# Kernel tuning notes

Measured on AMD Instinct MI355X. Metric: run time of the kernel, lower is better.

The kernel has to match this reference:

```python
import jax, jax.numpy as jnp
import numpy as np

N_SRC = 100000
N_DST = 100000
N_EDGES = 640000
D = 128
D_OUT = 128


def setup_inputs() -> dict:
    key = jax.random.key(0)
    k1, k2, k3, k4, k5, k6 = jax.random.split(key, 6)
    h_src = jax.random.normal(k1, (N_SRC, D), dtype=jnp.float32)
    h_dst = jax.random.normal(k2, (N_DST, D), dtype=jnp.float32)
    src_idx = jax.random.randint(k3, (N_EDGES,), 0, N_SRC, dtype=jnp.int32)
    dst_idx = jax.random.randint(k4, (N_EDGES,), 0, N_DST, dtype=jnp.int32)
    W = jax.random.normal(k5, (2 * D, D_OUT), dtype=jnp.float32) * 0.05
    b = jax.random.normal(k6, (D_OUT,), dtype=jnp.float32) * 0.05
    return {"h_src": h_src, "h_dst": h_dst, "src_idx": src_idx,
            "dst_idx": dst_idx, "W": W, "b": b}


def reference(h_src, h_dst, src_idx, dst_idx, W, b):
    # copy_u: gather source features along edges -> [E, D]
    msgs = h_src[src_idx]
    # mean aggregation per destination node (segment mean)
    summed = jax.ops.segment_sum(msgs, dst_idx, num_segments=N_DST)  # [N_dst, D]
    deg = jax.ops.segment_sum(jnp.ones((N_EDGES,), dtype=h_src.dtype),
                              dst_idx, num_segments=N_DST)  # [N_dst]
    h_N = summed / jnp.maximum(deg, 1.0)[:, None]
    # concat self + neighbor mean, then linear projection
    h_total = jnp.concatenate([h_dst, h_N], axis=1)  # [N_dst, 2D]
    return h_total @ W + b
```

## Files before the change

kernel.cpp:

```cpp
#include <hip/hip_runtime.h>

#define D 128
#define N_SRC 100000
#define N_DST 100000
#define N_EDGES 640000

#define SCAN_BLK 1024
#define N_SCAN_BLOCKS ((N_DST + SCAN_BLK - 1) / SCAN_BLK)

typedef __attribute__((ext_vector_type(8))) short s8v;
typedef __attribute__((ext_vector_type(4))) float f32x4;

__device__ __forceinline__ unsigned short f2bf(float f) {
    unsigned int u = __float_as_uint(f);
    u += 0x7fffu + ((u >> 16) & 1u);
    return (unsigned short)(u >> 16);
}


__global__ __launch_bounds__(256) void hist_kernel(
    const int* __restrict__ dst_idx, int* __restrict__ counts)
{
    int e = blockIdx.x * 256 + threadIdx.x;
    if (e < N_EDGES) atomicAdd(&counts[dst_idx[e]], 1);
}

__global__ __launch_bounds__(256) void scan_blocks(
    const int* __restrict__ counts, int* __restrict__ row_start,
    int* __restrict__ block_sums)
{
    __shared__ int sh[256];
    const int tid = threadIdx.x;
    const int base = blockIdx.x * SCAN_BLK + tid * 4;
    int v[4];
    int local = 0;
#pragma unroll
    for (int k = 0; k < 4; k++) {
        int idx = base + k;
        v[k] = (idx < N_DST) ? counts[idx] : 0;
        local += v[k];
    }
    sh[tid] = local;
    __syncthreads();
    for (int off = 1; off < 256; off <<= 1) {
        int t = (tid >= off) ? sh[tid - off] : 0;
        __syncthreads();
        sh[tid] += t;
        __syncthreads();
    }
    int run = (tid == 0) ? 0 : sh[tid - 1];
    if (tid == 255) block_sums[blockIdx.x] = sh[255];
#pragma unroll
    for (int k = 0; k < 4; k++) {
        int idx = base + k;
        if (idx < N_DST) row_start[idx] = run;
        run += v[k];
    }
}

__global__ __launch_bounds__(128) void scan_top(
    const int* __restrict__ block_sums, int* __restrict__ block_offsets)
{
    __shared__ int sh[128];
    const int tid = threadIdx.x;
    sh[tid] = (tid < N_SCAN_BLOCKS) ? block_sums[tid] : 0;
    __syncthreads();
    for (int off = 1; off < 128; off <<= 1) {
        int t = (tid >= off) ? sh[tid - off] : 0;
        __syncthreads();
        sh[tid] += t;
        __syncthreads();
    }
    if (tid < N_SCAN_BLOCKS) block_offsets[tid] = (tid == 0) ? 0 : sh[tid - 1];
}

__global__ __launch_bounds__(256) void add_offsets(
    int* __restrict__ row_start, const int* __restrict__ block_offsets,
    int* __restrict__ cursor)
{
    int i = blockIdx.x * 256 + threadIdx.x;
    if (i < N_DST) {
        int v = row_start[i] + block_offsets[i / SCAN_BLK];
        row_start[i] = v;
        cursor[i] = v;
    }
    if (i == 0) row_start[N_DST] = N_EDGES;
}

__global__ __launch_bounds__(256) void scatter_perm(
    const int* __restrict__ src_idx, const int* __restrict__ dst_idx,
    int* __restrict__ cursor, int* __restrict__ edge_src)
{
    int e = blockIdx.x * 256 + threadIdx.x;
    if (e < N_EDGES) {
        int d = dst_idx[e];
        int pos = atomicAdd(&cursor[d], 1);
        edge_src[pos] = src_idx[e];
    }
}

__global__ __launch_bounds__(256) void pack_W(
    const float* __restrict__ W, unsigned short* __restrict__ Bp)
{
    int id = blockIdx.x * 256 + threadIdx.x;
    if (id >= 32768) return;
    int j = id & 7;
    int l = (id >> 3) & 63;
    int t = (id >> 9) & 7;
    int s = id >> 12;
    int k = s * 32 + (l >> 4) * 8 + j;
    int n = t * 16 + (l & 15);
    Bp[id] = f2bf(W[k * D + n]);
}

__global__ __launch_bounds__(256) void aggregate(
    const float* __restrict__ h_src, const int* __restrict__ row_start,
    const int* __restrict__ edge_src, unsigned int* __restrict__ A32)
{
    const int wave = threadIdx.x >> 6;
    const int lane = threadIdx.x & 63;
    const int row = blockIdx.x * 4 + wave;
    if (row >= N_DST) return;
    const int start = row_start[row];
    const int deg = row_start[row + 1] - start;
    float2 acc = {0.f, 0.f};
    for (int base = 0; base < deg; base += 8) {
        int j = base + (lane & 7);
        int myid = edge_src[start + min(j, deg - 1)];
#pragma unroll
        for (int t = 0; t < 8; t++) {
            int s = __shfl(myid, t);
            float2 v = ((const float2*)(h_src + (size_t)s * D))[lane];
            bool ok = (base + t) < deg;
            acc.x += ok ? v.x : 0.f;
            acc.y += ok ? v.y : 0.f;
        }
    }
    const float inv = 1.0f / fmaxf((float)deg, 1.0f);
    unsigned int packed = (unsigned int)f2bf(acc.x * inv)
                        | ((unsigned int)f2bf(acc.y * inv) << 16);
    A32[(size_t)row * 128 + 64 + lane] = packed;
}

__global__ __launch_bounds__(256, 4) void mfma_gemm(
    const float* __restrict__ h_dst,
    const unsigned short* __restrict__ A,
    const unsigned short* __restrict__ Bp,
    const float* __restrict__ bias,
    float* __restrict__ out)
{
    const int wave = threadIdx.x >> 6;
    const int lane = threadIdx.x & 63;
    const int row0 = (blockIdx.x * 4 + wave) * 32;
    if (row0 >= N_DST) return;
    const int quad = lane >> 4;
    const int lr = lane & 15;
    const int r0 = row0 + lr;
    const int r1 = row0 + 16 + lr;

    f32x4 acc0[8], acc1[8];
#pragma unroll
    for (int t = 0; t < 8; t++) {
        acc0[t] = (f32x4){0.f, 0.f, 0.f, 0.f};
        acc1[t] = (f32x4){0.f, 0.f, 0.f, 0.f};
    }

    const float* p0 = h_dst + (size_t)r0 * D + quad * 8;
    const float* p1 = h_dst + (size_t)r1 * D + quad * 8;
    const unsigned short* q0 = A + (size_t)r0 * 256 + 128 + quad * 8;
    const unsigned short* q1 = A + (size_t)r1 * 256 + 128 + quad * 8;

#pragma unroll
    for (int s = 0; s < 4; s++) {
        float4 x0 = *(const float4*)(p0 + s * 32);
        float4 y0 = *(const float4*)(p0 + s * 32 + 4);
        float4 x1 = *(const float4*)(p1 + s * 32);
        float4 y1 = *(const float4*)(p1 + s * 32 + 4);
        unsigned short a0u[8], a1u[8];
        a0u[0]=f2bf(x0.x); a0u[1]=f2bf(x0.y); a0u[2]=f2bf(x0.z); a0u[3]=f2bf(x0.w);
        a0u[4]=f2bf(y0.x); a0u[5]=f2bf(y0.y); a0u[6]=f2bf(y0.z); a0u[7]=f2bf(y0.w);
        a1u[0]=f2bf(x1.x); a1u[1]=f2bf(x1.y); a1u[2]=f2bf(x1.z); a1u[3]=f2bf(x1.w);
        a1u[4]=f2bf(y1.x); a1u[5]=f2bf(y1.y); a1u[6]=f2bf(y1.z); a1u[7]=f2bf(y1.w);
        s8v a0 = *(s8v*)a0u;
        s8v a1 = *(s8v*)a1u;
#pragma unroll
        for (int t = 0; t < 8; t++) {
            s8v bf = *(const s8v*)(Bp + ((size_t)(s * 8 + t) * 64 + lane) * 8);
            acc0[t] = __builtin_amdgcn_mfma_f32_16x16x32_bf16(a0, bf, acc0[t], 0, 0, 0);
            acc1[t] = __builtin_amdgcn_mfma_f32_16x16x32_bf16(a1, bf, acc1[t], 0, 0, 0);
        }
    }
#pragma unroll
    for (int s = 4; s < 8; s++) {
        s8v a0 = *(const s8v*)(q0 + (s - 4) * 32);
        s8v a1 = *(const s8v*)(q1 + (s - 4) * 32);
#pragma unroll
        for (int t = 0; t < 8; t++) {
            s8v bf = *(const s8v*)(Bp + ((size_t)(s * 8 + t) * 64 + lane) * 8);
            acc0[t] = __builtin_amdgcn_mfma_f32_16x16x32_bf16(a0, bf, acc0[t], 0, 0, 0);
            acc1[t] = __builtin_amdgcn_mfma_f32_16x16x32_bf16(a1, bf, acc1[t], 0, 0, 0);
        }
    }

#pragma unroll
    for (int t = 0; t < 8; t++) {
        float bv = bias[t * 16 + lr];
#pragma unroll
        for (int r = 0; r < 4; r++) {
            int rowa = row0 + quad * 4 + r;
            int rowb = row0 + 16 + quad * 4 + r;
            out[(size_t)rowa * D + t * 16 + lr] = acc0[t][r] + bv;
            out[(size_t)rowb * D + t * 16 + lr] = acc1[t][r] + bv;
        }
    }
}

extern "C" void kernel_launch(void* const* d_in, const int* in_sizes, int n_in,
                              void* d_out, int out_size, void* d_ws, size_t ws_size,
                              hipStream_t stream) {
    const float* h_src  = (const float*)d_in[0];
    const float* h_dst  = (const float*)d_in[1];
    const int* src_idx  = (const int*)d_in[2];
    const int* dst_idx  = (const int*)d_in[3];
    const float* W      = (const float*)d_in[4];
    const float* b      = (const float*)d_in[5];
    float* out = (float*)d_out;

    unsigned short* Bp = (unsigned short*)d_ws;
    int* ws_i          = (int*)((char*)d_ws + 65536);
    int* row_start     = ws_i;
    int* cursor        = row_start + (N_DST + 1);
    int* counts        = cursor + N_DST;
    int* block_sums    = counts + N_DST;
    int* block_offsets = block_sums + N_SCAN_BLOCKS;
    int* edge_src      = block_offsets + N_SCAN_BLOCKS;

    hipMemsetAsync(counts, 0, (size_t)N_DST * sizeof(int), stream);

    hist_kernel<<<(N_EDGES + 255) / 256, 256, 0, stream>>>(dst_idx, counts);
    scan_blocks<<<N_SCAN_BLOCKS, 256, 0, stream>>>(counts, row_start, block_sums);
    scan_top<<<1, 128, 0, stream>>>(block_sums, block_offsets);
    add_offsets<<<(N_DST + 255) / 256, 256, 0, stream>>>(row_start, block_offsets, cursor);
    scatter_perm<<<(N_EDGES + 255) / 256, 256, 0, stream>>>(src_idx, dst_idx, cursor, edge_src);

    pack_W<<<128, 256, 0, stream>>>(W, Bp);

    aggregate<<<N_DST / 4, 256, 0, stream>>>(h_src, row_start, edge_src,
                                             (unsigned int*)d_out);

    int gemm_blocks = (N_DST / 32 + 3) / 4;
    mfma_gemm<<<gemm_blocks, 256, 0, stream>>>(
        h_dst, (const unsigned short*)d_out, Bp, b, out);
}
```

Baseline: 280.0 us.

## Pre-convert h_src to bf16 for gathers and fuse small setup kernels

Adds a prep kernel that converts h_src to bf16 into the first half of each output row, computes the destination histogram and packs W, all in one launch. Aggregation then gathers bf16 rows, halving gather bytes, and handles two rows per wave with 32-lane halves. The top-level scan is folded into add_offsets, which drops a launch. The cost is an extra full pass over h_src plus bf16 rounding of the neighbor inputs before summation, which adds precision error. The scratch space inside the output buffer now holds bf16 h_src rows until the GEMM overwrites them.

```diff
diff --git a/kernel.cpp b/kernel.cpp
--- a/kernel.cpp
+++ b/kernel.cpp
@@ -8,6 +8,10 @@
 #define SCAN_BLK 1024
 #define N_SCAN_BLOCKS ((N_DST + SCAN_BLK - 1) / SCAN_BLK)
 
+#define HIST_BLOCKS ((N_EDGES + 255) / 256)
+#define CVT_BLOCKS  ((N_SRC * D / 8) / 256)
+#define PACKW_BLOCKS 128
+
 typedef __attribute__((ext_vector_type(8))) short s8v;
 typedef __attribute__((ext_vector_type(4))) float f32x4;
 
@@ -17,13 +21,45 @@
     return (unsigned short)(u >> 16);
 }
 
-
-__global__ __launch_bounds__(256) void hist_kernel(
-    const int* __restrict__ dst_idx, int* __restrict__ counts)
-{
-    int e = blockIdx.x * 256 + threadIdx.x;
-    if (e < N_EDGES) atomicAdd(&counts[dst_idx[e]], 1);
-}
+__device__ __forceinline__ unsigned int pk2(float a, float b) {
+    return (unsigned int)f2bf(a) | ((unsigned int)f2bf(b) << 16);
+}
+
+__global__ __launch_bounds__(256) void prep(
+    const int* __restrict__ dst_idx, int* __restrict__ counts,
+    const float* __restrict__ h_src, unsigned int* __restrict__ A32,
+    const float* __restrict__ W, unsigned short* __restrict__ Bp)
+{
+    const int blk = blockIdx.x;
+    const int tid = threadIdx.x;
+    if (blk < HIST_BLOCKS) {
+        int e = blk * 256 + tid;
+        if (e < N_EDGES) atomicAdd(&counts[dst_idx[e]], 1);
+    } else if (blk < HIST_BLOCKS + CVT_BLOCKS) {
+        int id = (blk - HIST_BLOCKS) * 256 + tid;
+        size_t e = (size_t)id * 8;
+        const float4* p = (const float4*)(h_src + e);
+        float4 x = p[0], y = p[1];
+        uint4 o;
+        o.x = pk2(x.x, x.y); o.y = pk2(x.z, x.w);
+        o.z = pk2(y.x, y.y); o.w = pk2(y.z, y.w);
+        int r = id >> 4;
+        int c = (id & 15) * 8;
+        *(uint4*)(A32 + (size_t)r * 128 + (c >> 1)) = o;
+    } else {
+        int id = (blk - HIST_BLOCKS - CVT_BLOCKS) * 256 + tid;
+        if (id < 32768) {
+            int j = id & 7;
+            int l = (id >> 3) & 63;
+            int t = (id >> 9) & 7;
+            int s = id >> 12;
+            int k = s * 32 + (l >> 4) * 8 + j;
+            int n = t * 16 + (l & 15);
+            Bp[id] = f2bf(W[k * D + n]);
+        }
+    }
+}
+
 
 __global__ __launch_bounds__(256) void scan_blocks(
     const int* __restrict__ counts, int* __restrict__ row_start,
@@ -58,29 +94,25 @@
     }
 }
 
-__global__ __launch_bounds__(128) void scan_top(
-    const int* __restrict__ block_sums, int* __restrict__ block_offsets)
+__global__ __launch_bounds__(256) void add_offsets(
+    int* __restrict__ row_start, const int* __restrict__ block_sums,
+    int* __restrict__ cursor)
 {
     __shared__ int sh[128];
     const int tid = threadIdx.x;
-    sh[tid] = (tid < N_SCAN_BLOCKS) ? block_sums[tid] : 0;
+    if (tid < 128) sh[tid] = (tid < N_SCAN_BLOCKS) ? block_sums[tid] : 0;
     __syncthreads();
     for (int off = 1; off < 128; off <<= 1) {
-        int t = (tid >= off) ? sh[tid - off] : 0;
-        __syncthreads();
-        sh[tid] += t;
-        __syncthreads();
-    }
-    if (tid < N_SCAN_BLOCKS) block_offsets[tid] = (tid == 0) ? 0 : sh[tid - 1];
-}
-
-__global__ __launch_bounds__(256) void add_offsets(
-    int* __restrict__ row_start, const int* __restrict__ block_offsets,
-    int* __restrict__ cursor)
-{
-    int i = blockIdx.x * 256 + threadIdx.x;
+        int t = (tid < 128 && tid >= off) ? sh[tid - off] : 0;
+        __syncthreads();
+        if (tid < 128) sh[tid] += t;
+        __syncthreads();
+    }
+    int i = blockIdx.x * 256 + tid;
     if (i < N_DST) {
-        int v = row_start[i] + block_offsets[i / SCAN_BLK];
+        int blk = i / SCAN_BLK;
+        int off = (blk == 0) ? 0 : sh[blk - 1];
+        int v = row_start[i] + off;
         row_start[i] = v;
         cursor[i] = v;
     }
@@ -99,47 +131,37 @@
     }
 }
 
-__global__ __launch_bounds__(256) void pack_W(
-    const float* __restrict__ W, unsigned short* __restrict__ Bp)
-{
-    int id = blockIdx.x * 256 + threadIdx.x;
-    if (id >= 32768) return;
-    int j = id & 7;
-    int l = (id >> 3) & 63;
-    int t = (id >> 9) & 7;
-    int s = id >> 12;
-    int k = s * 32 + (l >> 4) * 8 + j;
-    int n = t * 16 + (l & 15);
-    Bp[id] = f2bf(W[k * D + n]);
-}
-
 __global__ __launch_bounds__(256) void aggregate(
-    const float* __restrict__ h_src, const int* __restrict__ row_start,
+    const unsigned short* __restrict__ hs16,
+    const int* __restrict__ row_start,
     const int* __restrict__ edge_src, unsigned int* __restrict__ A32)
 {
     const int wave = threadIdx.x >> 6;
-    const int lane = threadIdx.x & 63;
-    const int row = blockIdx.x * 4 + wave;
-    if (row >= N_DST) return;
+    const int half = (threadIdx.x >> 5) & 1;
+    const int hl = threadIdx.x & 31;
+    const int row = blockIdx.x * 8 + wave * 2 + half;
     const int start = row_start[row];
     const int deg = row_start[row + 1] - start;
-    float2 acc = {0.f, 0.f};
+    f32x4 acc = {0.f, 0.f, 0.f, 0.f};
     for (int base = 0; base < deg; base += 8) {
-        int j = base + (lane & 7);
+        int j = base + (hl & 7);
         int myid = edge_src[start + min(j, deg - 1)];
 #pragma unroll
         for (int t = 0; t < 8; t++) {
-            int s = __shfl(myid, t);
-            float2 v = ((const float2*)(h_src + (size_t)s * D))[lane];
-            bool ok = (base + t) < deg;
-            acc.x += ok ? v.x : 0.f;
-            acc.y += ok ? v.y : 0.f;
+            int s = __shfl(myid, t, 32);
+            uint2 u = *(const uint2*)(hs16 + (size_t)s * 256 + hl * 4);
+            float m = ((base + t) < deg) ? 1.f : 0.f;
+            acc.x = fmaf(__uint_as_float(u.x << 16), m, acc.x);
+            acc.y = fmaf(__uint_as_float(u.x & 0xffff0000u), m, acc.y);
+            acc.z = fmaf(__uint_as_float(u.y << 16), m, acc.z);
+            acc.w = fmaf(__uint_as_float(u.y & 0xffff0000u), m, acc.w);
         }
     }
     const float inv = 1.0f / fmaxf((float)deg, 1.0f);
-    unsigned int packed = (unsigned int)f2bf(acc.x * inv)
-                        | ((unsigned int)f2bf(acc.y * inv) << 16);
-    A32[(size_t)row * 128 + 64 + lane] = packed;
+    uint2 o;
+    o.x = pk2(acc.x * inv, acc.y * inv);
+    o.y = pk2(acc.z * inv, acc.w * inv);
+    *(uint2*)(A32 + (size_t)row * 128 + 64 + hl * 2) = o;
 }
 
 __global__ __launch_bounds__(256, 4) void mfma_gemm(
@@ -232,21 +254,19 @@
     int* cursor        = row_start + (N_DST + 1);
     int* counts        = cursor + N_DST;
     int* block_sums    = counts + N_DST;
-    int* block_offsets = block_sums + N_SCAN_BLOCKS;
-    int* edge_src      = block_offsets + N_SCAN_BLOCKS;
+    int* edge_src      = block_sums + N_SCAN_BLOCKS;
 
     hipMemsetAsync(counts, 0, (size_t)N_DST * sizeof(int), stream);
 
-    hist_kernel<<<(N_EDGES + 255) / 256, 256, 0, stream>>>(dst_idx, counts);
+    prep<<<HIST_BLOCKS + CVT_BLOCKS + PACKW_BLOCKS, 256, 0, stream>>>(
+        dst_idx, counts, h_src, (unsigned int*)d_out, W, Bp);
+
     scan_blocks<<<N_SCAN_BLOCKS, 256, 0, stream>>>(counts, row_start, block_sums);
-    scan_top<<<1, 128, 0, stream>>>(block_sums, block_offsets);
-    add_offsets<<<(N_DST + 255) / 256, 256, 0, stream>>>(row_start, block_offsets, cursor);
+    add_offsets<<<(N_DST + 255) / 256, 256, 0, stream>>>(row_start, block_sums, cursor);
     scatter_perm<<<(N_EDGES + 255) / 256, 256, 0, stream>>>(src_idx, dst_idx, cursor, edge_src);
 
-    pack_W<<<128, 256, 0, stream>>>(W, Bp);
-
-    aggregate<<<N_DST / 4, 256, 0, stream>>>(h_src, row_start, edge_src,
-                                             (unsigned int*)d_out);
+    aggregate<<<N_DST / 8, 256, 0, stream>>>(
+        (const unsigned short*)d_out, row_start, edge_src, (unsigned int*)d_out);
 
     int gemm_blocks = (N_DST / 32 + 3) / 4;
     mfma_gemm<<<gemm_blocks, 256, 0, stream>>>(
```

Measured after the change: 262.0 us. -6.4%, faster.
